# Kernel tuning notes

Hardware: AMD Instinct MI355X
Metric: run time of the kernel (lower is better)

The kernel has to match this reference:

```python
import jax, jax.numpy as jnp
import numpy as np

PRECS = 1e-05
# HBV parameter scaling bounds (order: BETA, FC, K0, K1, K2, LP, PERC, UZL, TT, CFMAX, CFR, CWH, BETAET)
LB = jnp.array([1.0, 50.0, 0.05, 0.01, 0.001, 0.2, 0.0, 0.0, -2.5, 0.5, 0.0, 0.0, 0.3], dtype=jnp.float32)
UB = jnp.array([6.0, 1000.0, 0.9, 0.5, 0.2, 1.0, 10.0, 100.0, 2.5, 10.0, 0.1, 0.2, 5.0], dtype=jnp.float32)

NSTEP, NGRID, MU = 730, 1000, 8

def setup_inputs() -> dict:
    key = jax.random.key(0)
    k1, k2, k3, k4 = jax.random.split(key, 4)
    P = jax.random.uniform(k1, (NSTEP, NGRID), jnp.float32) * 10.0      # precip mm/day
    T = jax.random.normal(k2, (NSTEP, NGRID), jnp.float32) * 8.0 + 2.0  # temp degC
    ET = jax.random.uniform(k3, (NSTEP, NGRID), jnp.float32) * 5.0      # PET mm/day
    x = jnp.stack([P, T, ET], axis=-1)                                   # [Nstep, Ngrid, 3]
    parameters = jax.random.uniform(k4, (NSTEP, NGRID, 13, MU), jnp.float32)  # raw in [0,1]
    tdlst = jnp.arange(2, dtype=jnp.int32)  # -> param indices {12, 0} = BETAET, BETA dynamic
    return {"x": x, "parameters": parameters, "staind": NSTEP - 1, "tdlst": tdlst, "mu": MU}

def _hbv_forward(x, parameters, staind, tdlst):
    # scale raw params to physical ranges: [Nstep, Ngrid, 13, mu]
    parT = LB[None, None, :, None] + parameters * (UB - LB)[None, None, :, None]
    # static params taken from time index staind, broadcast over time
    parhbv = jnp.broadcast_to(parT[staind][None], parT.shape)
    # dynamic params: dydrop=0 -> bernoulli mask is all zeros -> comPar = dynPar
    idx = jnp.mod(jnp.asarray(tdlst) - 1, 13)
    parhbv = parhbv.at[:, :, idx, :].set(parT[:, :, idx, :])

    Ngrid = x.shape[1]
    mu = parameters.shape[-1]
    init = tuple(jnp.full((Ngrid, mu), 0.001, dtype=jnp.float32) for _ in range(5))

    def step(carry, inp):
        SP, MW, SM, SUZ, SLZ = carry
        P_, T_, ET_, par = inp              # P_/T_/ET_: [Ngrid], par: [Ngrid, 13, mu]
        P_, T_, ET_ = P_[:, None], T_[:, None], ET_[:, None]
        BETA, FC, K0, K1, K2, LP, PERCc, UZL, TT, CFMAX, CFR, CWH, BETAET = (
            par[:, i] for i in range(13))
        is_rain = (T_ >= TT).astype(jnp.float32)
        RAIN = P_ * is_rain
        SNOW = P_ * (1.0 - is_rain)
        SP = SP + SNOW
        melt = jnp.minimum(jnp.maximum(CFMAX * (T_ - TT), 0.0), SP)
        MW = MW + melt
        SP = SP - melt
        refr = jnp.minimum(jnp.maximum(CFR * CFMAX * (TT - T_), 0.0), MW)
        SP = SP + refr
        MW = MW - refr
        tosoil = jnp.maximum(MW - CWH * SP, 0.0)
        MW = MW - tosoil
        soil_wetness = jnp.clip((SM / FC) ** BETA, 0.0, 1.0)
        recharge = (RAIN + tosoil) * soil_wetness
        SM = SM + RAIN + tosoil - recharge
        excess = jnp.maximum(SM - FC, 0.0)
        SM = SM - excess
        evapfactor = jnp.clip((SM / (LP * FC)) ** BETAET, 0.0, 1.0)
        ETact = jnp.minimum(SM, ET_ * evapfactor)
        SM = jnp.maximum(SM - ETact, PRECS)
        SUZ = SUZ + recharge + excess
        PERC = jnp.minimum(SUZ, PERCc)
        SUZ = SUZ - PERC
        Q0 = K0 * jnp.maximum(SUZ - UZL, 0.0)
        SUZ = SUZ - Q0
        Q1 = K1 * SUZ
        SUZ = SUZ - Q1
        SLZ = SLZ + PERC
        Q2 = K2 * SLZ
        SLZ = SLZ - Q2
        return (SP, MW, SM, SUZ, SLZ), Q0 + Q1 + Q2

    _, Qsimmu = jax.lax.scan(step, init, (x[:, :, 0], x[:, :, 1], x[:, :, 2], parhbv))
    # muwts=None -> mean over components; routOpt=False -> Qs = Qsimave[..., None]
    return Qsimmu.mean(-1)[..., None]  # [Nstep, Ngrid, 1]

def reference(x, parameters, staind, tdlst, mu):
    return _hbv_forward(x, parameters, staind, tdlst)
```

## Files before the change

### kernel.cpp

```cpp
#include <hip/hip_runtime.h>

#define NSTEP 730
#define NGRID 1000
#define NPAR  13
#define PRECS 1e-5f

#define PAR_TSTRIDE 104000u
#define PAR_GSTRIDE 104u
#define X_TSTRIDE 3000u

#define G10   10
#define NG10  73

#define GSTEPS 10
#define NGROUP 73

#define LDS_PREP_BUF 5760
#define LDS_QL_BASE  11520
#define LDS_QL_BUF   640
#define LDS_TOTAL    12800

constexpr float LB_[NPAR] = {1.0f, 50.0f, 0.05f, 0.01f, 0.001f, 0.2f, 0.0f,
                             0.0f, -2.5f, 0.5f, 0.0f, 0.0f, 0.3f};
constexpr float UB_[NPAR] = {6.0f, 1000.0f, 0.9f, 0.5f, 0.2f, 1.0f, 10.0f,
                             100.0f, 2.5f, 10.0f, 0.1f, 0.2f, 5.0f};

__device__ __forceinline__ float fast_rcp(float x)  { return __builtin_amdgcn_rcpf(x); }
__device__ __forceinline__ float fast_exp2(float x) { return __builtin_amdgcn_exp2f(x); }
__device__ __forceinline__ float fast_log2(float x) { return __builtin_amdgcn_logf(x); }

__device__ __forceinline__ int mod13(int v) {
    int r = v % NPAR;
    if (r < 0) r += NPAR;
    return r;
}

template <int CTRL>
__device__ __forceinline__ float dpp_xadd(float v) {
    int r = __builtin_amdgcn_update_dpp(0, __float_as_int(v), CTRL, 0xF, 0xF, true);
    return v + __int_as_float(r);
}
__device__ __forceinline__ float mu8_sum(float v) {
    v = dpp_xadd<0xB1>(v);
    v = dpp_xadd<0x4E>(v);
    int s = __builtin_amdgcn_ds_swizzle(__float_as_int(v), 0x101F);
    return v + __int_as_float(s);
}

__device__ __forceinline__ float hbv_step_core(
    float P_, float T_, float ET_,
    float BETA, float FC, float K0, float K1, float K2,
    float PERCc, float UZL, float TT, float CFMAX, float CFR, float CWH,
    float BETAET, float rcpFC, float rcpLPFC,
    float& SP, float& MW, float& SM, float& SUZ, float& SLZ)
{
    float dT    = T_ - TT;
    float RAIN  = (T_ >= TT) ? P_ : 0.f;
    float SNOW  = P_ - RAIN;
    SP += SNOW;
    float cm    = CFMAX * dT;
    float melt  = fminf(fmaxf(cm, 0.f), SP);
    MW += melt; SP -= melt;
    float refr  = fminf(fmaxf(-CFR * cm, 0.f), MW);
    SP += refr; MW -= refr;
    float tosoil = fmaxf(MW - CWH * SP, 0.f);
    MW -= tosoil;
    float soilw  = fminf(fast_exp2(BETA * fast_log2(SM * rcpFC)), 1.f);
    float rt     = RAIN + tosoil;
    float rech   = rt * soilw;
    SM += rt - rech;
    float excess = fmaxf(SM - FC, 0.f);
    SM -= excess;
    float evapf  = fminf(fast_exp2(BETAET * fast_log2(SM * rcpLPFC)), 1.f);
    float ETact  = fminf(SM, ET_ * evapf);
    SM = fmaxf(SM - ETact, PRECS);
    SUZ += rech + excess;
    float PERC = fminf(SUZ, PERCc);
    SUZ -= PERC;
    float Q0 = K0 * fmaxf(SUZ - UZL, 0.f);
    SUZ -= Q0;
    float Q1 = K1 * SUZ;
    SUZ -= Q1;
    SLZ += PERC;
    float Q2 = K2 * SLZ;
    SLZ -= Q2;
    return Q0 + Q1 + Q2;
}

__device__ void hbv_generic2(
    const float* __restrict__ x, const float* __restrict__ par,
    int staind, int idx0, int idx1, float* __restrict__ out, int g, int m)
{
    const unsigned cpar = (unsigned)g * PAR_GSTRIDE + (unsigned)m;
    const unsigned g3   = (unsigned)g * 3u;

    float lb0 = 0.f, dv0 = 0.f, lb1 = 0.f, dv1 = 0.f;
    float sel0[NPAR], sel1[NPAR];
#pragma unroll
    for (int i = 0; i < NPAR; ++i) {
        sel0[i] = (idx0 == i) ? 1.f : 0.f;
        sel1[i] = (idx1 == i && idx1 != idx0) ? 1.f : 0.f;
        if (idx0 == i) { lb0 = LB_[i]; dv0 = UB_[i] - LB_[i]; }
        if (idx1 == i) { lb1 = LB_[i]; dv1 = UB_[i] - LB_[i]; }
    }
    const unsigned off0 = (unsigned)idx0 * 8u, off1 = (unsigned)idx1 * 8u;

    float basep[NPAR];
    const unsigned sbase = (unsigned)staind * PAR_TSTRIDE + cpar;
#pragma unroll
    for (int i = 0; i < NPAR; ++i) {
        float fxv = fmaf(par[sbase + (unsigned)i * 8u], UB_[i] - LB_[i], LB_[i]);
        basep[i] = fxv * (1.f - sel0[i] - sel1[i]);
    }

    float bP[2][GSTEPS], bT[2][GSTEPS], bEv[2][GSTEPS];
    float bS0[2][GSTEPS], bS1[2][GSTEPS];
    float SP = 0.001f, MW = 0.001f, SM = 0.001f, SUZ = 0.001f, SLZ = 0.001f;

    auto load = [&](int b, int t0) {
#pragma unroll
        for (int j = 0; j < GSTEPS; ++j) {
            unsigned t  = (unsigned)(t0 + j);
            unsigned xo = t * X_TSTRIDE + g3;
            bP[b][j]  = x[xo];
            bT[b][j]  = x[xo + 1u];
            bEv[b][j] = x[xo + 2u];
            unsigned po = t * PAR_TSTRIDE + cpar;
            bS0[b][j] = par[po + off0];
            bS1[b][j] = par[po + off1];
        }
    };
    auto compute = [&](int b, int t0) {
        float ql[GSTEPS];
#pragma unroll
        for (int j = 0; j < GSTEPS; ++j) {
            float sv0 = fmaf(bS0[b][j], dv0, lb0);
            float sv1 = fmaf(bS1[b][j], dv1, lb1);
            float pr[NPAR];
#pragma unroll
            for (int i = 0; i < NPAR; ++i)
                pr[i] = fmaf(sel1[i], sv1, fmaf(sel0[i], sv0, basep[i]));
            float rcpFC   = fast_rcp(pr[1]);
            float rcpLPFC = fast_rcp(pr[5] * pr[1]);
            ql[j] = hbv_step_core(bP[b][j], bT[b][j], bEv[b][j],
                                  pr[0], pr[1], pr[2], pr[3], pr[4], pr[6],
                                  pr[7], pr[8], pr[9], pr[10], pr[11], pr[12],
                                  rcpFC, rcpLPFC, SP, MW, SM, SUZ, SLZ);
        }
#pragma unroll
        for (int j = 0; j < GSTEPS; ++j) {
            float s = mu8_sum(ql[j]);
            if (m == 0)
                out[(unsigned)(t0 + j) * (unsigned)NGRID + (unsigned)g] = s * 0.125f;
        }
    };

    load(0, 0);
    for (int gp = 0; gp < NGROUP; gp += 2) {
        if (gp + 1 < NGROUP) load(1, (gp + 1) * GSTEPS);
        compute(0, gp * GSTEPS);
        if (gp + 2 < NGROUP) load(0, (gp + 2) * GSTEPS);
        if (gp + 1 < NGROUP) compute(1, (gp + 1) * GSTEPS);
    }
}

__global__ __launch_bounds__(128, 1) void hbv_pc(
    const float* __restrict__ x, const float* __restrict__ par,
    const int* __restrict__ staind_p, const int* __restrict__ tdlst_p,
    float* __restrict__ out)
{
    __shared__ float lds[LDS_TOTAL];

    const int lane  = threadIdx.x & 63;
    const int wave  = threadIdx.x >> 6;
    const int chain = blockIdx.x * 64 + lane;
    const int g = chain >> 3;
    const int m = chain & 7;

    const int staind = __builtin_amdgcn_readfirstlane(staind_p[0]);
    const int idx0   = __builtin_amdgcn_readfirstlane(mod13(tdlst_p[0] - 1));
    const int idx1   = __builtin_amdgcn_readfirstlane(mod13(tdlst_p[1] - 1));

    if (!(idx0 == 12 && idx1 == 0)) {
        if (wave == 0) hbv_generic2(x, par, staind, idx0, idx1, out, g, m);
        return;
    }

    const unsigned cpar = (unsigned)g * PAR_GSTRIDE + (unsigned)m;
    const unsigned g3   = (unsigned)g * 3u;

    float fx[NPAR];
    const unsigned sbase = (unsigned)staind * PAR_TSTRIDE + cpar;
#pragma unroll
    for (int i = 0; i < NPAR; ++i)
        fx[i] = fmaf(par[sbase + (unsigned)i * 8u], UB_[i] - LB_[i], LB_[i]);

    if (wave == 0) {
        const float TT = fx[8], CFMAX = fx[9], CC = fx[10] * fx[9];
        const float rcpFC    = fast_rcp(fx[1]);
        const float rcpLPFC  = fast_rcp(fx[5] * fx[1]);
        const float l2rcpFC  = fast_log2(rcpFC);
        const float l2rcpLPF = fast_log2(rcpLPFC);
        constexpr float lbB = LB_[0],  dvB = UB_[0]  - LB_[0];
        constexpr float lbE = LB_[12], dvE = UB_[12] - LB_[12];

        float vP[3][G10], vT[3][G10], vE[3][G10], v0[3][G10], v1[3][G10];

        auto gload = [&](int b, int grp) {
            int t0 = grp * G10;
#pragma unroll
            for (int j = 0; j < G10; ++j) {
                unsigned t  = (unsigned)(t0 + j);
                unsigned xo = t * X_TSTRIDE + g3;
                vP[b][j] = x[xo];
                vT[b][j] = x[xo + 1u];
                vE[b][j] = x[xo + 2u];
                unsigned po = t * PAR_TSTRIDE + cpar;
                v0[b][j] = par[po + 96u];
                v1[b][j] = par[po];
            }
        };
        auto prep = [&](int b, int dbuf) {
            float* pw = &lds[dbuf * LDS_PREP_BUF + lane];
#pragma unroll
            for (int j = 0; j < G10; ++j) {
                float Pj = vP[b][j], Tj = vT[b][j];
                float dT   = Tj - TT;
                float RAIN = (dT >= 0.f) ? Pj : 0.f;
                float BETAET = fmaf(v0[b][j], dvE, lbE);
                float BETA   = fmaf(v1[b][j], dvB, lbB);
                pw[(j * 9 + 0) * 64] = Pj - RAIN;
                pw[(j * 9 + 1) * 64] = fmaxf(CFMAX * dT, 0.f);
                pw[(j * 9 + 2) * 64] = fmaxf(-CC * dT, 0.f);
                pw[(j * 9 + 3) * 64] = RAIN;
                pw[(j * 9 + 4) * 64] = vE[b][j];
                pw[(j * 9 + 5) * 64] = BETA * l2rcpFC;
                pw[(j * 9 + 6) * 64] = BETAET * l2rcpLPF;
                pw[(j * 9 + 7) * 64] = BETA;
                pw[(j * 9 + 8) * 64] = BETAET;
            }
        };
        auto red = [&](int sbuf, int grp) {
            const float* qb = &lds[LDS_QL_BASE + sbuf * LDS_QL_BUF + lane];
            float s[G10];
#pragma unroll
            for (int j = 0; j < G10; ++j) s[j] = mu8_sum(qb[j * 64]);
            if (m == 0) {
#pragma unroll
                for (int j = 0; j < G10; ++j)
                    out[(unsigned)(grp * G10 + j) * (unsigned)NGRID + (unsigned)g]
                        = s[j] * 0.125f;
            }
        };

#define PHASE(kk, BL, BP)                                   \
        {                                                   \
            __syncthreads();                                \
            if ((kk) + 3 < NG10) gload(BL, (kk) + 3);       \
            if ((kk) + 1 < NG10) prep(BP, ((kk) + 1) & 1);  \
            if ((kk) >= 1) red(((kk) - 1) & 1, (kk) - 1);   \
        }

        gload(0, 0); gload(1, 1); gload(2, 2);
        prep(0, 0);
        int k = 0;
        for (int t = 0; t < 24; ++t) {
            PHASE(k, 0, 1); ++k;
            PHASE(k, 1, 2); ++k;
            PHASE(k, 2, 0); ++k;
        }
        PHASE(k, 0, 1);
        __syncthreads();
        red(0, 72);
#undef PHASE
    } else {
        const float FC = fx[1], K0 = fx[2], K1 = fx[3], K2 = fx[4],
                    PERCc = fx[6], UZL = fx[7], CWH = fx[11];
        float SP = 0.001f, MW = 0.001f, SM = 0.001f, SUZ = 0.001f, SLZ = 0.001f;

        for (int k = 0; k < NG10; ++k) {
            __syncthreads();
            const float* pr = &lds[(k & 1) * LDS_PREP_BUF + lane];
            float* qw = &lds[LDS_QL_BASE + (k & 1) * LDS_QL_BUF + lane];
#pragma unroll
            for (int j = 0; j < G10; ++j) {
                float SNOW   = pr[(j * 9 + 0) * 64];
                float MAXCM  = pr[(j * 9 + 1) * 64];
                float MAXRF  = pr[(j * 9 + 2) * 64];
                float RAIN   = pr[(j * 9 + 3) * 64];
                float ET     = pr[(j * 9 + 4) * 64];
                float bbc    = pr[(j * 9 + 5) * 64];
                float ebc    = pr[(j * 9 + 6) * 64];
                float BETA   = pr[(j * 9 + 7) * 64];
                float BETAET = pr[(j * 9 + 8) * 64];

                SP += SNOW;
                float melt = fminf(MAXCM, SP);
                MW += melt; SP -= melt;
                float refr = fminf(MAXRF, MW);
                SP += refr; MW -= refr;
                float tosoil = fmaxf(fmaf(-CWH, SP, MW), 0.f);
                MW -= tosoil;
                float rt    = RAIN + tosoil;
                float soilw = fast_exp2(fmaf(BETA, fast_log2(SM), bbc));
                float rech  = rt * soilw;
                float SM_mid = SM + rt - rech;
                float SM_ae  = fminf(SM_mid, FC);
                float excess = SM_mid - SM_ae;
                float evapf  = fminf(fast_exp2(fmaf(BETAET, fast_log2(SM_ae), ebc)), 1.f);
                SM = fmaxf(fmaf(-ET, evapf, SM_ae), PRECS);
                SUZ += rech + excess;
                float PERC = fminf(SUZ, PERCc);
                float SUZp = SUZ - PERC;
                float Q0   = K0 * fmaxf(SUZp - UZL, 0.f);
                float SUZq = SUZp - Q0;
                float Q1   = K1 * SUZq;
                SUZ = SUZq - Q1;
                SLZ += PERC;
                float Q2 = K2 * SLZ;
                SLZ -= Q2;
                qw[j * 64] = (Q0 + Q1) + Q2;
            }
        }
        __syncthreads();
    }
}

__global__ __launch_bounds__(64, 1) void hbv_scan_generic(
    const float* __restrict__ x, const float* __restrict__ par,
    const int* __restrict__ staind_p, const int* __restrict__ tdlst_p,
    int n_td, float* __restrict__ out)
{
    const int tid = blockIdx.x * 64 + threadIdx.x;
    const int g   = tid >> 3;
    const int m   = tid & 7;
    if (g >= NGRID) return;

    const int staind    = staind_p[0];
    const unsigned cpar = (unsigned)g * PAR_GSTRIDE + (unsigned)m;
    const unsigned g3   = (unsigned)g * 3u;

    unsigned off[NPAR], st[NPAR];
#pragma unroll
    for (int i = 0; i < NPAR; ++i) {
        bool vr = false;
        for (int j = 0; j < n_td; ++j)
            if (mod13(tdlst_p[j] - 1) == i) vr = true;
        off[i] = (vr ? 0u : (unsigned)staind * PAR_TSTRIDE) + cpar + (unsigned)i * 8u;
        st[i]  = vr ? PAR_TSTRIDE : 0u;
    }

    float SP = 0.001f, MW = 0.001f, SM = 0.001f, SUZ = 0.001f, SLZ = 0.001f;
    for (int t = 0; t < NSTEP; ++t) {
        unsigned xo = (unsigned)t * X_TSTRIDE + g3;
        float P_ = x[xo], T_ = x[xo + 1u], E_ = x[xo + 2u];
        float pr[NPAR];
#pragma unroll
        for (int i = 0; i < NPAR; ++i) {
            pr[i] = fmaf(par[off[i]], UB_[i] - LB_[i], LB_[i]);
            off[i] += st[i];
        }
        float rcpFC   = fast_rcp(pr[1]);
        float rcpLPFC = fast_rcp(pr[5] * pr[1]);
        float q = hbv_step_core(P_, T_, E_, pr[0], pr[1], pr[2], pr[3], pr[4],
                                pr[6], pr[7], pr[8], pr[9], pr[10], pr[11],
                                pr[12], rcpFC, rcpLPFC, SP, MW, SM, SUZ, SLZ);
        float s = mu8_sum(q);
        if (m == 0) out[(unsigned)t * (unsigned)NGRID + (unsigned)g] = s * 0.125f;
    }
}

extern "C" void kernel_launch(void* const* d_in, const int* in_sizes, int n_in,
                              void* d_out, int out_size, void* d_ws, size_t ws_size,
                              hipStream_t stream) {
    const float* x      = (const float*)d_in[0];
    const float* par    = (const float*)d_in[1];
    const int*   staind = (const int*)d_in[2];
    const int*   tdlst  = (const int*)d_in[3];
    float*       out    = (float*)d_out;
    const int n_td = in_sizes[3];

    if (n_td == 2) {
        hbv_pc<<<125, 128, 0, stream>>>(x, par, staind, tdlst, out);
    } else {
        hbv_scan_generic<<<125, 64, 0, stream>>>(x, par, staind, tdlst,
                                                 n_td, out);
    }
}
```

Baseline: 421.3 us.

## Merge producer/consumer waves into single-wave kernel with register-buffered loads

Replaces the two-wave LDS producer/consumer scheme with one 64-lane wave per block. That wave triple-buffers global loads in registers, computes the forcing terms inline, and writes outputs directly. The mu-reduction now uses a DPP row_half_mirror step instead of ds_swizzle. This removes the per-group __syncthreads barriers and the LDS round-trips on the serial recurrence. In exchange, the preparation ALU work and load issue now share a wave with the latency-bound chain, and register pressure rises.

Measured after the change: 450.4 us. 6.9% more time.

```diff
diff --git a/kernel.cpp b/kernel.cpp
--- a/kernel.cpp
+++ b/kernel.cpp
@@ -14,11 +14,6 @@
 
 #define GSTEPS 10
 #define NGROUP 73
-
-#define LDS_PREP_BUF 5760
-#define LDS_QL_BASE  11520
-#define LDS_QL_BUF   640
-#define LDS_TOTAL    12800
 
 constexpr float LB_[NPAR] = {1.0f, 50.0f, 0.05f, 0.01f, 0.001f, 0.2f, 0.0f,
                              0.0f, -2.5f, 0.5f, 0.0f, 0.0f, 0.3f};
@@ -45,6 +40,12 @@
     v = dpp_xadd<0x4E>(v);
     int s = __builtin_amdgcn_ds_swizzle(__float_as_int(v), 0x101F);
     return v + __int_as_float(s);
+}
+__device__ __forceinline__ float mu8_sum_dpp(float v) {
+    v = dpp_xadd<0xB1>(v);
+    v = dpp_xadd<0x4E>(v);
+    v = dpp_xadd<0x141>(v);
+    return v;
 }
 
 __device__ __forceinline__ float hbv_step_core(
@@ -164,15 +165,12 @@
     }
 }
 
-__global__ __launch_bounds__(128, 1) void hbv_pc(
+__global__ __launch_bounds__(64, 1) void hbv_fast(
     const float* __restrict__ x, const float* __restrict__ par,
     const int* __restrict__ staind_p, const int* __restrict__ tdlst_p,
     float* __restrict__ out)
 {
-    __shared__ float lds[LDS_TOTAL];
-
-    const int lane  = threadIdx.x & 63;
-    const int wave  = threadIdx.x >> 6;
+    const int lane  = threadIdx.x;
     const int chain = blockIdx.x * 64 + lane;
     const int g = chain >> 3;
     const int m = chain & 7;
@@ -182,7 +180,7 @@
     const int idx1   = __builtin_amdgcn_readfirstlane(mod13(tdlst_p[1] - 1));
 
     if (!(idx0 == 12 && idx1 == 0)) {
-        if (wave == 0) hbv_generic2(x, par, staind, idx0, idx1, out, g, m);
+        hbv_generic2(x, par, staind, idx0, idx1, out, g, m);
         return;
     }
 
@@ -195,135 +193,95 @@
     for (int i = 0; i < NPAR; ++i)
         fx[i] = fmaf(par[sbase + (unsigned)i * 8u], UB_[i] - LB_[i], LB_[i]);
 
-    if (wave == 0) {
-        const float TT = fx[8], CFMAX = fx[9], CC = fx[10] * fx[9];
-        const float rcpFC    = fast_rcp(fx[1]);
-        const float rcpLPFC  = fast_rcp(fx[5] * fx[1]);
-        const float l2rcpFC  = fast_log2(rcpFC);
-        const float l2rcpLPF = fast_log2(rcpLPFC);
-        constexpr float lbB = LB_[0],  dvB = UB_[0]  - LB_[0];
-        constexpr float lbE = LB_[12], dvE = UB_[12] - LB_[12];
-
-        float vP[3][G10], vT[3][G10], vE[3][G10], v0[3][G10], v1[3][G10];
-
-        auto gload = [&](int b, int grp) {
-            int t0 = grp * G10;
-#pragma unroll
-            for (int j = 0; j < G10; ++j) {
-                unsigned t  = (unsigned)(t0 + j);
-                unsigned xo = t * X_TSTRIDE + g3;
-                vP[b][j] = x[xo];
-                vT[b][j] = x[xo + 1u];
-                vE[b][j] = x[xo + 2u];
-                unsigned po = t * PAR_TSTRIDE + cpar;
-                v0[b][j] = par[po + 96u];
-                v1[b][j] = par[po];
-            }
-        };
-        auto prep = [&](int b, int dbuf) {
-            float* pw = &lds[dbuf * LDS_PREP_BUF + lane];
-#pragma unroll
-            for (int j = 0; j < G10; ++j) {
-                float Pj = vP[b][j], Tj = vT[b][j];
-                float dT   = Tj - TT;
-                float RAIN = (dT >= 0.f) ? Pj : 0.f;
-                float BETAET = fmaf(v0[b][j], dvE, lbE);
-                float BETA   = fmaf(v1[b][j], dvB, lbB);
-                pw[(j * 9 + 0) * 64] = Pj - RAIN;
-                pw[(j * 9 + 1) * 64] = fmaxf(CFMAX * dT, 0.f);
-                pw[(j * 9 + 2) * 64] = fmaxf(-CC * dT, 0.f);
-                pw[(j * 9 + 3) * 64] = RAIN;
-                pw[(j * 9 + 4) * 64] = vE[b][j];
-                pw[(j * 9 + 5) * 64] = BETA * l2rcpFC;
-                pw[(j * 9 + 6) * 64] = BETAET * l2rcpLPF;
-                pw[(j * 9 + 7) * 64] = BETA;
-                pw[(j * 9 + 8) * 64] = BETAET;
-            }
-        };
-        auto red = [&](int sbuf, int grp) {
-            const float* qb = &lds[LDS_QL_BASE + sbuf * LDS_QL_BUF + lane];
-            float s[G10];
-#pragma unroll
-            for (int j = 0; j < G10; ++j) s[j] = mu8_sum(qb[j * 64]);
-            if (m == 0) {
-#pragma unroll
-                for (int j = 0; j < G10; ++j)
-                    out[(unsigned)(grp * G10 + j) * (unsigned)NGRID + (unsigned)g]
-                        = s[j] * 0.125f;
-            }
-        };
-
-#define PHASE(kk, BL, BP)                                   \
-        {                                                   \
-            __syncthreads();                                \
-            if ((kk) + 3 < NG10) gload(BL, (kk) + 3);       \
-            if ((kk) + 1 < NG10) prep(BP, ((kk) + 1) & 1);  \
-            if ((kk) >= 1) red(((kk) - 1) & 1, (kk) - 1);   \
-        }
-
-        gload(0, 0); gload(1, 1); gload(2, 2);
-        prep(0, 0);
-        int k = 0;
-        for (int t = 0; t < 24; ++t) {
-            PHASE(k, 0, 1); ++k;
-            PHASE(k, 1, 2); ++k;
-            PHASE(k, 2, 0); ++k;
-        }
-        PHASE(k, 0, 1);
-        __syncthreads();
-        red(0, 72);
-#undef PHASE
-    } else {
-        const float FC = fx[1], K0 = fx[2], K1 = fx[3], K2 = fx[4],
-                    PERCc = fx[6], UZL = fx[7], CWH = fx[11];
-        float SP = 0.001f, MW = 0.001f, SM = 0.001f, SUZ = 0.001f, SLZ = 0.001f;
-
-        for (int k = 0; k < NG10; ++k) {
-            __syncthreads();
-            const float* pr = &lds[(k & 1) * LDS_PREP_BUF + lane];
-            float* qw = &lds[LDS_QL_BASE + (k & 1) * LDS_QL_BUF + lane];
-#pragma unroll
-            for (int j = 0; j < G10; ++j) {
-                float SNOW   = pr[(j * 9 + 0) * 64];
-                float MAXCM  = pr[(j * 9 + 1) * 64];
-                float MAXRF  = pr[(j * 9 + 2) * 64];
-                float RAIN   = pr[(j * 9 + 3) * 64];
-                float ET     = pr[(j * 9 + 4) * 64];
-                float bbc    = pr[(j * 9 + 5) * 64];
-                float ebc    = pr[(j * 9 + 6) * 64];
-                float BETA   = pr[(j * 9 + 7) * 64];
-                float BETAET = pr[(j * 9 + 8) * 64];
-
-                SP += SNOW;
-                float melt = fminf(MAXCM, SP);
-                MW += melt; SP -= melt;
-                float refr = fminf(MAXRF, MW);
-                SP += refr; MW -= refr;
-                float tosoil = fmaxf(fmaf(-CWH, SP, MW), 0.f);
-                MW -= tosoil;
-                float rt    = RAIN + tosoil;
-                float soilw = fast_exp2(fmaf(BETA, fast_log2(SM), bbc));
-                float rech  = rt * soilw;
-                float SM_mid = SM + rt - rech;
-                float SM_ae  = fminf(SM_mid, FC);
-                float excess = SM_mid - SM_ae;
-                float evapf  = fminf(fast_exp2(fmaf(BETAET, fast_log2(SM_ae), ebc)), 1.f);
-                SM = fmaxf(fmaf(-ET, evapf, SM_ae), PRECS);
-                SUZ += rech + excess;
-                float PERC = fminf(SUZ, PERCc);
-                float SUZp = SUZ - PERC;
-                float Q0   = K0 * fmaxf(SUZp - UZL, 0.f);
-                float SUZq = SUZp - Q0;
-                float Q1   = K1 * SUZq;
-                SUZ = SUZq - Q1;
-                SLZ += PERC;
-                float Q2 = K2 * SLZ;
-                SLZ -= Q2;
-                qw[j * 64] = (Q0 + Q1) + Q2;
-            }
-        }
-        __syncthreads();
-    }
+    const float FC = fx[1], K0 = fx[2], K1 = fx[3], K2 = fx[4],
+                PERCc = fx[6], UZL = fx[7], TT = fx[8], CFMAX = fx[9],
+                CWH = fx[11];
+    const float CC       = fx[10] * fx[9];
+    const float rcpFC    = fast_rcp(fx[1]);
+    const float rcpLPFC  = fast_rcp(fx[5] * fx[1]);
+    const float l2rcpFC  = fast_log2(rcpFC);
+    const float l2rcpLPF = fast_log2(rcpLPFC);
+    constexpr float lbB = LB_[0],  dvB = UB_[0]  - LB_[0];
+    constexpr float lbE = LB_[12], dvE = UB_[12] - LB_[12];
+
+    float vP[3][G10], vT[3][G10], vE[3][G10], v0[3][G10], v1[3][G10];
+
+    struct F3 { float a, b, c; };
+
+    auto gload = [&](int b, int grp) {
+        const int t0 = grp * G10;
+        const float* xp = x   + (unsigned)t0 * X_TSTRIDE  + g3;
+        const float* pp = par + (unsigned)t0 * PAR_TSTRIDE + cpar;
+#pragma unroll
+        for (int j = 0; j < G10; ++j) {
+            F3 xv = *reinterpret_cast<const F3*>(xp);
+            vP[b][j] = xv.a; vT[b][j] = xv.b; vE[b][j] = xv.c;
+            v1[b][j] = pp[0];
+            v0[b][j] = pp[96];
+            xp += X_TSTRIDE;
+            pp += PAR_TSTRIDE;
+        }
+    };
+
+    float SP = 0.001f, MW = 0.001f, SM = 0.001f, SUZ = 0.001f, SLZ = 0.001f;
+
+    auto compute = [&](int b, int grp) {
+        const int t0 = grp * G10;
+#pragma unroll
+        for (int j = 0; j < G10; ++j) {
+            float Pj = vP[b][j], Tj = vT[b][j], ET = vE[b][j];
+            float dT     = Tj - TT;
+            float RAIN   = (dT >= 0.f) ? Pj : 0.f;
+            float SNOW   = Pj - RAIN;
+            float MAXCM  = fmaxf(CFMAX * dT, 0.f);
+            float MAXRF  = fmaxf(-CC * dT, 0.f);
+            float BETAET = fmaf(v0[b][j], dvE, lbE);
+            float BETA   = fmaf(v1[b][j], dvB, lbB);
+            float bbc    = BETA * l2rcpFC;
+            float ebc    = BETAET * l2rcpLPF;
+
+            SP += SNOW;
+            float melt = fminf(MAXCM, SP);
+            MW += melt; SP -= melt;
+            float refr = fminf(MAXRF, MW);
+            SP += refr; MW -= refr;
+            float tosoil = fmaxf(fmaf(-CWH, SP, MW), 0.f);
+            MW -= tosoil;
+            float rt    = RAIN + tosoil;
+            float soilw = fast_exp2(fmaf(BETA, fast_log2(SM), bbc));
+            float rech  = rt * soilw;
+            float SM_mid = SM + rt - rech;
+            float SM_ae  = fminf(SM_mid, FC);
+            float excess = SM_mid - SM_ae;
+            float evapf  = fminf(fast_exp2(fmaf(BETAET, fast_log2(SM_ae), ebc)), 1.f);
+            SM = fmaxf(fmaf(-ET, evapf, SM_ae), PRECS);
+            SUZ += rech + excess;
+            float PERC = fminf(SUZ, PERCc);
+            float SUZp = SUZ - PERC;
+            float Q0   = K0 * fmaxf(SUZp - UZL, 0.f);
+            float SUZq = SUZp - Q0;
+            float Q1   = K1 * SUZq;
+            SUZ = SUZq - Q1;
+            SLZ += PERC;
+            float Q2 = K2 * SLZ;
+            SLZ -= Q2;
+            float q = (Q0 + Q1) + Q2;
+
+            float s = mu8_sum_dpp(q);
+            if (m == 0)
+                out[(unsigned)(t0 + j) * (unsigned)NGRID + (unsigned)g]
+                    = s * 0.125f;
+        }
+    };
+
+    gload(0, 0); gload(1, 1); gload(2, 2);
+    int k = 0;
+    for (int t = 0; t < 24; ++t) {
+        compute(0, k); if (k + 3 < NG10) gload(0, k + 3); ++k;
+        compute(1, k); if (k + 3 < NG10) gload(1, k + 3); ++k;
+        compute(2, k); if (k + 3 < NG10) gload(2, k + 3); ++k;
+    }
+    compute(0, 72);
 }
 
 __global__ __launch_bounds__(64, 1) void hbv_scan_generic(
@@ -381,7 +339,7 @@
     const int n_td = in_sizes[3];
 
     if (n_td == 2) {
-        hbv_pc<<<125, 128, 0, stream>>>(x, par, staind, tdlst, out);
+        hbv_fast<<<125, 64, 0, stream>>>(x, par, staind, tdlst, out);
     } else {
         hbv_scan_generic<<<125, 64, 0, stream>>>(x, par, staind, tdlst,
                                                  n_td, out);
```
